# Optimization experiments

Hardware: AMD Instinct MI355X
Metric: run time of the kernel (lower is better)

## Reference

```python
import jax, jax.numpy as jnp
import numpy as np
from jax import lax

K = 25
SIGMA = 9.0
PAD = K // 2


def _gaussian_kernel():
    # 1D gaussian, normalized, then outer product -> depthwise (3,1,K,K) kernel
    coords = jnp.arange(K, dtype=jnp.float32) - (K // 2)
    g = jnp.exp(-coords ** 2 / (2.0 * SIGMA ** 2))
    g = g / g.sum()
    k2d = jnp.outer(g, g)  # (K, K)
    return jnp.broadcast_to(k2d[None, None], (3, 1, K, K))


def setup_inputs() -> dict:
    key = jax.random.key(0)
    x = jax.random.uniform(key, (32, 3, 512, 512), dtype=jnp.float32)
    return {"x": x}


def reference(x):
    kernel = _gaussian_kernel()
    y = lax.conv_general_dilated(
        x, kernel,
        window_strides=(1, 1),
        padding=[(PAD, PAD), (PAD, PAD)],
        dimension_numbers=("NCHW", "OIHW", "NCHW"),
        feature_group_count=3,
    )
    return jnp.clip(y, 0.0, 1.0)
```

## Files before the change

kernel.cpp:

```cpp
#include <hip/hip_runtime.h>

#define NB 32
#define CC 3
#define HH 512
#define WW 512
#define KS 25
#define PAD 12
#define HT 8
#define LDSW 536

__device__ __forceinline__ float clamp01(float v) {
    return fminf(fmaxf(v, 0.0f), 1.0f);
}

template<bool EDGE>
__device__ __forceinline__ void blur_body(const float* __restrict__ ibase,
                                          float* __restrict__ obase,
                                          int r0, int tid, float* tile) {
    constexpr float W[KS] = {
        0.02181520f, 0.02514307f, 0.02862302f, 0.03218484f, 0.03574584f,
        0.03921371f, 0.04249020f, 0.04547544f, 0.04807347f, 0.05019624f,
        0.05176967f, 0.05273727f, 0.05306384f, 0.05273727f, 0.05176967f,
        0.05019624f, 0.04807347f, 0.04547544f, 0.04249020f, 0.03921371f,
        0.03574584f, 0.03218484f, 0.02862302f, 0.02514307f, 0.02181520f};

    if (tid < HT * 2 * PAD) {
        int r = tid / (2 * PAD);
        int k = tid - r * (2 * PAD);
        tile[r * LDSW + (k < PAD ? k : 512 + k)] = 0.0f;
    }

    const float* ip = ibase + tid * 2;
    float2 acc[HT];
#pragma unroll
    for (int j = 0; j < HT; ++j) acc[j] = make_float2(0.f, 0.f);

#pragma unroll
    for (int r = 0; r < HT + KS - 1; ++r) {
        int rr = r0 - PAD + r;
        float2 v = make_float2(0.f, 0.f);
        if (!EDGE || (rr >= 0 && rr < HH))
            v = *(const float2*)(ip + (long)rr * WW);
#pragma unroll
        for (int j = 0; j < HT; ++j) {
            int t = r - j;
            if (t >= 0 && t < KS) {
                acc[j].x += v.x * W[t];
                acc[j].y += v.y * W[t];
            }
        }
    }
#pragma unroll
    for (int j = 0; j < HT; ++j)
        *(float2*)&tile[j * LDSW + PAD + tid * 2] = acc[j];

    __syncthreads();

#pragma unroll
    for (int it = 0; it < 4; ++it) {
        int f = it * 256 + tid;
        int c4 = f & 127;
        int row = f >> 7;
        const float* lp = &tile[row * LDSW + c4 * 4];
        float o0 = 0.f, o1 = 0.f, o2 = 0.f, o3 = 0.f;
#pragma unroll
        for (int q = 0; q < 7; ++q) {
            float4 v = *(const float4*)(lp + 4 * q);
            float vv[4] = {v.x, v.y, v.z, v.w};
#pragma unroll
            for (int e = 0; e < 4; ++e) {
                int wdx = 4 * q + e;
                if (wdx - 0 >= 0 && wdx - 0 < KS) o0 += vv[e] * W[wdx];
                if (wdx - 1 >= 0 && wdx - 1 < KS) o1 += vv[e] * W[wdx - 1];
                if (wdx - 2 >= 0 && wdx - 2 < KS) o2 += vv[e] * W[wdx - 2];
                if (wdx - 3 >= 0 && wdx - 3 < KS) o3 += vv[e] * W[wdx - 3];
            }
        }
        float4 ov = make_float4(clamp01(o0), clamp01(o1), clamp01(o2), clamp01(o3));
        *(float4*)(obase + (long)(r0 + row) * WW + c4 * 4) = ov;
    }
}

__global__ __launch_bounds__(256, 4) void gblur_fused(const float* __restrict__ x,
                                                      float* __restrict__ out) {
    __shared__ float tile[HT * LDSW];

    int tid = threadIdx.x;

    int b = blockIdx.x;
    const int nwg = NB * CC * (HH / HT);
    int per = nwg >> 3;
    int swz = (b & 7) * per + (b >> 3);
    int plane = swz >> 6;
    int strip = swz & 63;
    int r0 = strip * HT;

    const float* ibase = x + (long)plane * (HH * WW);
    float*       obase = out + (long)plane * (HH * WW);

    if (r0 >= PAD && r0 <= HH - HT - PAD)
        blur_body<false>(ibase, obase, r0, tid, tile);
    else
        blur_body<true>(ibase, obase, r0, tid, tile);
}

extern "C" void kernel_launch(void* const* d_in, const int* in_sizes, int n_in,
                              void* d_out, int out_size, void* d_ws, size_t ws_size,
                              hipStream_t stream) {
    const float* x = (const float*)d_in[0];
    float* out = (float*)d_out;
    const int nwg = NB * CC * (HH / HT);
    gblur_fused<<<nwg, 256, 0, stream>>>(x, out);
}
```

Baseline: 43.61 us.

## Use packed fp16 dot2 for both blur passes with half-precision LDS tile

Converts input row pairs to packed fp16 and accumulates the vertical pass with v_dot2 instructions in fp32 accumulators. The horizontal pass then works from a half-width fp16 LDS tile, with each thread producing 8 outputs via dot2. This is meant to halve the FMA instruction count and the LDS footprint and traffic. The cost is fp16 rounding of inputs, weights and intermediates, which may increase error against the fp32 reference.

```diff
diff --git a/kernel.cpp b/kernel.cpp
--- a/kernel.cpp
+++ b/kernel.cpp
@@ -7,7 +7,26 @@
 #define KS 25
 #define PAD 12
 #define HT 8
-#define LDSW 536
+#define LDSW2 268
+
+typedef __fp16 h2 __attribute__((ext_vector_type(2)));
+
+#if __has_builtin(__builtin_amdgcn_fdot2)
+#define FDOT2(a, b, c) __builtin_amdgcn_fdot2((a), (b), (c), false)
+#else
+#define FDOT2(a, b, c) ((float)(a).x * (float)(b).x + (float)(a).y * (float)(b).y + (c))
+#endif
+
+__device__ constexpr float Wf[KS] = {
+    0.02181520f, 0.02514307f, 0.02862302f, 0.03218484f, 0.03574584f,
+    0.03921371f, 0.04249020f, 0.04547544f, 0.04807347f, 0.05019624f,
+    0.05176967f, 0.05273727f, 0.05306384f, 0.05273727f, 0.05176967f,
+    0.05019624f, 0.04807347f, 0.04547544f, 0.04249020f, 0.03921371f,
+    0.03574584f, 0.03218484f, 0.02862302f, 0.02514307f, 0.02181520f};
+
+__device__ constexpr float Wget(int t) {
+    return (t >= 0 && t < KS) ? Wf[t] : 0.0f;
+}
 
 __device__ __forceinline__ float clamp01(float v) {
     return fminf(fmaxf(v, 0.0f), 1.0f);
@@ -16,74 +35,83 @@
 template<bool EDGE>
 __device__ __forceinline__ void blur_body(const float* __restrict__ ibase,
                                           float* __restrict__ obase,
-                                          int r0, int tid, float* tile) {
-    constexpr float W[KS] = {
-        0.02181520f, 0.02514307f, 0.02862302f, 0.03218484f, 0.03574584f,
-        0.03921371f, 0.04249020f, 0.04547544f, 0.04807347f, 0.05019624f,
-        0.05176967f, 0.05273727f, 0.05306384f, 0.05273727f, 0.05176967f,
-        0.05019624f, 0.04807347f, 0.04547544f, 0.04249020f, 0.03921371f,
-        0.03574584f, 0.03218484f, 0.02862302f, 0.02514307f, 0.02181520f};
-
-    if (tid < HT * 2 * PAD) {
-        int r = tid / (2 * PAD);
-        int k = tid - r * (2 * PAD);
-        tile[r * LDSW + (k < PAD ? k : 512 + k)] = 0.0f;
+                                          int r0, int tid, unsigned* tile16) {
+    if (tid < HT * 12) {
+        int r = tid / 12;
+        int k = tid - r * 12;
+        tile16[r * LDSW2 + (k < 6 ? k : 256 + k)] = 0u;
     }
 
     const float* ip = ibase + tid * 2;
-    float2 acc[HT];
+    float accx[HT], accy[HT];
 #pragma unroll
-    for (int j = 0; j < HT; ++j) acc[j] = make_float2(0.f, 0.f);
+    for (int j = 0; j < HT; ++j) { accx[j] = 0.f; accy[j] = 0.f; }
 
 #pragma unroll
-    for (int r = 0; r < HT + KS - 1; ++r) {
-        int rr = r0 - PAD + r;
-        float2 v = make_float2(0.f, 0.f);
-        if (!EDGE || (rr >= 0 && rr < HH))
-            v = *(const float2*)(ip + (long)rr * WW);
+    for (int k = 0; k < 16; ++k) {
+        int rr0 = r0 - PAD + 2 * k;
+        int rr1 = rr0 + 1;
+        float2 va = make_float2(0.f, 0.f), vb = make_float2(0.f, 0.f);
+        if (!EDGE || (rr0 >= 0 && rr0 < HH)) va = *(const float2*)(ip + (long)rr0 * WW);
+        if (!EDGE || (rr1 >= 0 && rr1 < HH)) vb = *(const float2*)(ip + (long)rr1 * WW);
+        h2 px = __builtin_amdgcn_cvt_pkrtz(va.x, vb.x);
+        h2 py = __builtin_amdgcn_cvt_pkrtz(va.y, vb.y);
 #pragma unroll
         for (int j = 0; j < HT; ++j) {
-            int t = r - j;
-            if (t >= 0 && t < KS) {
-                acc[j].x += v.x * W[t];
-                acc[j].y += v.y * W[t];
+            const int t0 = 2 * k - j;
+            if (t0 >= -1 && t0 <= 24) {
+                const h2 wp = {(__fp16)Wget(t0), (__fp16)Wget(t0 + 1)};
+                accx[j] = FDOT2(px, wp, accx[j]);
+                accy[j] = FDOT2(py, wp, accy[j]);
             }
         }
     }
 #pragma unroll
-    for (int j = 0; j < HT; ++j)
-        *(float2*)&tile[j * LDSW + PAD + tid * 2] = acc[j];
+    for (int j = 0; j < HT; ++j) {
+        h2 w = __builtin_amdgcn_cvt_pkrtz(accx[j], accy[j]);
+        tile16[j * LDSW2 + 6 + tid] = __builtin_bit_cast(unsigned, w);
+    }
 
     __syncthreads();
 
 #pragma unroll
-    for (int it = 0; it < 4; ++it) {
+    for (int it = 0; it < 2; ++it) {
         int f = it * 256 + tid;
-        int c4 = f & 127;
-        int row = f >> 7;
-        const float* lp = &tile[row * LDSW + c4 * 4];
-        float o0 = 0.f, o1 = 0.f, o2 = 0.f, o3 = 0.f;
+        int g = f & 63;
+        int row = f >> 6;
+        const unsigned* lp = &tile16[row * LDSW2 + 4 * g];
+        h2 pa[16];
 #pragma unroll
-        for (int q = 0; q < 7; ++q) {
-            float4 v = *(const float4*)(lp + 4 * q);
-            float vv[4] = {v.x, v.y, v.z, v.w};
+        for (int q = 0; q < 4; ++q) {
+            uint4 c = *(const uint4*)(lp + 4 * q);
+            pa[4 * q + 0] = __builtin_bit_cast(h2, c.x);
+            pa[4 * q + 1] = __builtin_bit_cast(h2, c.y);
+            pa[4 * q + 2] = __builtin_bit_cast(h2, c.z);
+            pa[4 * q + 3] = __builtin_bit_cast(h2, c.w);
+        }
+        float res[8];
 #pragma unroll
-            for (int e = 0; e < 4; ++e) {
-                int wdx = 4 * q + e;
-                if (wdx - 0 >= 0 && wdx - 0 < KS) o0 += vv[e] * W[wdx];
-                if (wdx - 1 >= 0 && wdx - 1 < KS) o1 += vv[e] * W[wdx - 1];
-                if (wdx - 2 >= 0 && wdx - 2 < KS) o2 += vv[e] * W[wdx - 2];
-                if (wdx - 3 >= 0 && wdx - 3 < KS) o3 += vv[e] * W[wdx - 3];
+        for (int j = 0; j < 8; ++j) {
+            float o = 0.f;
+#pragma unroll
+            for (int m = 0; m < 16; ++m) {
+                const int t0 = 2 * m - j;
+                if (t0 >= -1 && t0 <= 24) {
+                    const h2 wp = {(__fp16)Wget(t0), (__fp16)Wget(t0 + 1)};
+                    o = FDOT2(pa[m], wp, o);
+                }
             }
+            res[j] = clamp01(o);
         }
-        float4 ov = make_float4(clamp01(o0), clamp01(o1), clamp01(o2), clamp01(o3));
-        *(float4*)(obase + (long)(r0 + row) * WW + c4 * 4) = ov;
+        float* op = obase + (long)(r0 + row) * WW + 8 * g;
+        *(float4*)(op + 0) = make_float4(res[0], res[1], res[2], res[3]);
+        *(float4*)(op + 4) = make_float4(res[4], res[5], res[6], res[7]);
     }
 }
 
 __global__ __launch_bounds__(256, 4) void gblur_fused(const float* __restrict__ x,
                                                       float* __restrict__ out) {
-    __shared__ float tile[HT * LDSW];
+    __shared__ unsigned tile16[HT * LDSW2];
 
     int tid = threadIdx.x;
 
@@ -99,9 +127,9 @@
     float*       obase = out + (long)plane * (HH * WW);
 
     if (r0 >= PAD && r0 <= HH - HT - PAD)
-        blur_body<false>(ibase, obase, r0, tid, tile);
+        blur_body<false>(ibase, obase, r0, tid, tile16);
     else
-        blur_body<true>(ibase, obase, r0, tid, tile);
+        blur_body<true>(ibase, obase, r0, tid, tile16);
 }
 
 extern "C" void kernel_launch(void* const* d_in, const int* in_sizes, int n_in,
```

Result: faster. 41.94 us (-3.8%).
